# Optimization experiments

Hardware: AMD Instinct MI355X
Metric: run time of the kernel (lower is better)

## Reference

```python
import jax, jax.numpy as jnp
import numpy as np

B, L, D, K = 64, 1024, 128, 256
SQRT_2D = float(np.sqrt(2 * D))


def _biamlp(x1, x2, Wi, bi, Wq, bq):
    # proj to 2*D, norm-weighted fusion, avg-pool(2)*2 (== pairwise sum), L2-normalize over dim 1
    f1 = x1 @ Wi + bi          # [B, L, 2D]
    f2 = x2 @ Wq + bq          # [B, L, 2D]
    n1 = jnp.linalg.norm(f1)   # global L2 norm (scalar), as torch.norm(., p=2)
    n2 = jnp.linalg.norm(f2)
    e = (n1 / (n1 + n2)) * f1 + (n2 / (n1 + n2)) * f2
    b, l, c = e.shape
    z = e.reshape(b, l, c // 2, 2).mean(-1) * 2.0   # AvgPool1d(2,2) * 2 -> [B, L, D]
    denom = jnp.maximum(jnp.linalg.norm(z, axis=1, keepdims=True), 1e-12)  # F.normalize dim=1
    return z / denom


def _branch(feats, G_src, W_aff, W_c, W_lin, W_h):
    # feats: [B, L, D]; G_src: [B, L, 2D] (tensor fed to the affine projection)
    # a_j = affine(G_src^T): [B, 2D, L] @ [L, L]
    a_j = jnp.einsum('blc,lm->bcm', G_src, W_aff)            # [B, 2D, L]
    att = jnp.einsum('bld,bcl->bdc', feats, a_j) / SQRT_2D    # [B, D, 2D]
    C = jnp.tanh(att)
    H = jax.nn.relu(C @ W_c + jnp.einsum('bld,lk->bdk', feats, W_lin))  # [B, D, K]
    out = jnp.swapaxes(H @ W_h, 1, 2) + feats                 # [B, L, D]
    return out


def setup_inputs() -> dict:
    key = jax.random.key(0)
    ks = jax.random.split(key, 22)
    s = 0.02
    inp = {
        'f1_norm': jax.random.normal(ks[0], (B, L, D), jnp.float32),
        'f2_norm': jax.random.normal(ks[1], (B, L, D), jnp.float32),
        'f3_norm': jax.random.normal(ks[2], (B, L, D), jnp.float32),
        # BiAMLP params (feat_size = 128)
        'Wi': jax.random.normal(ks[3], (D, 2 * D), jnp.float32) * s,
        'bi': jax.random.normal(ks[4], (2 * D,), jnp.float32) * s,
        'Wq': jax.random.normal(ks[5], (D, 2 * D), jnp.float32) * s,
        'bq': jax.random.normal(ks[6], (2 * D,), jnp.float32) * s,
        # affine_{a,v,l}: Linear(l, l, bias=False), stored [in, out]
        'Wa_aff': jax.random.normal(ks[7], (L, L), jnp.float32) * s,
        'Wv_aff': jax.random.normal(ks[8], (L, L), jnp.float32) * s,
        'Wl_aff': jax.random.normal(ks[9], (L, L), jnp.float32) * s,
        # W_{a,v,t}: Linear(l, k)
        'W_a': jax.random.normal(ks[10], (L, K), jnp.float32) * s,
        'W_v': jax.random.normal(ks[11], (L, K), jnp.float32) * s,
        'W_t': jax.random.normal(ks[12], (L, K), jnp.float32) * s,
        # W_c{a,v,t}: Linear(2d, k)
        'W_ca': jax.random.normal(ks[13], (2 * D, K), jnp.float32) * s,
        'W_cv': jax.random.normal(ks[14], (2 * D, K), jnp.float32) * s,
        'W_ct': jax.random.normal(ks[15], (2 * D, K), jnp.float32) * s,
        # W_h{a,v,t}: Linear(k, l)
        'W_ha': jax.random.normal(ks[16], (K, L), jnp.float32) * s,
        'W_hv': jax.random.normal(ks[17], (K, L), jnp.float32) * s,
        'W_ht': jax.random.normal(ks[18], (K, L), jnp.float32) * s,
    }
    return inp


def reference(f1_norm, f2_norm, f3_norm, Wi, bi, Wq, bq, Wa_aff, Wv_aff, Wl_aff,
              W_a, W_v, W_t, W_ca, W_cv, W_ct, W_ha, W_hv, W_ht):
    txt, aud, vis = f1_norm, f2_norm, f3_norm
    # G2 = mode(txt, vis) and G3 = mode(aud, vis) are computed but unused in the
    # original (dead code); only G = G1 affects the output.
    G = _biamlp(txt, aud, Wi, bi, Wq, bq)        # [B, L, D]
    G_ag = jnp.concatenate([aud, G], axis=2)     # [B, L, 2D]
    G_lg = jnp.concatenate([txt, G], axis=2)     # [B, L, 2D]
    # NOTE: original bug preserved -- the visual branch projects G_ag (not G_vg).
    aud_out = _branch(aud, G_ag, Wa_aff, W_ca, W_a, W_ha)
    vis_out = _branch(vis, G_ag, Wv_aff, W_cv, W_v, W_hv)
    txt_out = _branch(txt, G_lg, Wl_aff, W_ct, W_t, W_ht)
    return (txt_out, aud_out, vis_out)
```

## Files before the change

### kernel.cpp

```cpp
#include <hip/hip_runtime.h>
#include <math.h>

typedef __attribute__((ext_vector_type(8))) short bf16x8;
typedef __attribute__((ext_vector_type(4))) float f32x4;

static constexpr int B_ = 64, L_ = 1024, D_ = 128, K_ = 256;
static constexpr long BLD_ = (long)B_ * L_ * D_;
static constexpr long LD_  = (long)L_ * D_;

__device__ __forceinline__ unsigned short f2b(float f) {
    unsigned int u = __builtin_bit_cast(unsigned int, f);
    u = (u + 0x7fffu + ((u >> 16) & 1u)) >> 16;
    return (unsigned short)u;
}
__device__ __forceinline__ float b2f(unsigned short h) {
    unsigned int u = ((unsigned int)h) << 16;
    return __builtin_bit_cast(float, u);
}

__device__ __forceinline__ void gl16(const unsigned short* g, unsigned short* s) {
    __builtin_amdgcn_global_load_lds(
        (const __attribute__((address_space(1))) unsigned int*)g,
        (__attribute__((address_space(3))) unsigned int*)s, 16, 0, 0);
}

struct TrEnt { const float* src; unsigned short* dst; int R, C, tr, start; };
struct TrTab { TrEnt e[17]; };

__global__ __launch_bounds__(256)
void trk(TrTab tab)
{
    __shared__ unsigned short T[64][72];
    int bid = blockIdx.x;
    int ei = 0;
    #pragma unroll
    for (int i = 1; i < 17; ++i) if (bid >= tab.e[i].start) ei = i;
    TrEnt e = tab.e[ei];
    int tile = bid - e.start;
    int ntR = e.R >> 6, ntC = e.C >> 6;
    int nt = ntR * ntC;
    int bb = tile / nt, tt = tile - bb * nt;
    int ri = tt % ntR, ci = tt / ntR;
    const float* src = e.src + (long)bb * e.R * e.C + (long)(ri * 64) * e.C + ci * 64;
    int t = threadIdx.x;
    if (!e.tr) {
        unsigned short* dstd = e.dst + (long)bb * e.R * e.C + (long)(ri * 64) * e.C + ci * 64;
        int r = t >> 2, cq = t & 3;
        const float* s = src + (long)r * e.C + cq * 16;
        unsigned short tmp[16];
        #pragma unroll
        for (int f = 0; f < 4; ++f) {
            float4 v = *(const float4*)(s + f * 4);
            tmp[f*4+0]=f2b(v.x); tmp[f*4+1]=f2b(v.y); tmp[f*4+2]=f2b(v.z); tmp[f*4+3]=f2b(v.w);
        }
        unsigned short* dp = dstd + (long)r * e.C + cq * 16;
        *(uint4*)&dp[0] = *(uint4*)&tmp[0];
        *(uint4*)&dp[8] = *(uint4*)&tmp[8];
        return;
    }
    unsigned short* dst = e.dst + (long)bb * e.R * e.C + (long)(ci * 64) * e.R + ri * 64;
    {
        int r = t >> 2, cq = t & 3;
        const float* s = src + (long)r * e.C + cq * 16;
        unsigned short tmp[16];
        #pragma unroll
        for (int f = 0; f < 4; ++f) {
            float4 v = *(const float4*)(s + f * 4);
            tmp[f*4+0]=f2b(v.x); tmp[f*4+1]=f2b(v.y); tmp[f*4+2]=f2b(v.z); tmp[f*4+3]=f2b(v.w);
        }
        *(uint4*)&T[r][cq*16]   = *(uint4*)&tmp[0];
        *(uint4*)&T[r][cq*16+8] = *(uint4*)&tmp[8];
    }
    __syncthreads();
    {
        int cr = t >> 2, rq = t & 3;
        unsigned short tmp[16];
        #pragma unroll
        for (int j = 0; j < 16; ++j) tmp[j] = T[rq*16 + j][cr];
        unsigned short* dp = dst + (long)cr * e.R + rq * 16;
        *(uint4*)&dp[0] = *(uint4*)&tmp[0];
        *(uint4*)&dp[8] = *(uint4*)&tmp[8];
    }
}

struct OpDesc {
    const unsigned short* A;
    long aOff0, aOff1, aOff2, sA;
    int lda;
    const unsigned short* B0;
    long bOff0, bOff1, bOff2, sB0;
    const unsigned short* B1;
    long sB1;
    int ldb;
    void* C;
    long sC;
    int ldc;
    const float* E0; const float* E1; const float* E2;
    float* ss;
    int Kd;
};

template<int EPI, int AF32, int TM>
__device__ __forceinline__ void gbody(const OpDesc& d, int bx, int by, int zrem,
                                      unsigned short (*As)[TM][32],
                                      unsigned short (*Bs)[128][32])
{
    const int tid = threadIdx.x;
    const long m0 = (long)bx * TM;
    const int n0 = by * 128;
    const int br = zrem >> 6, bb = zrem & 63;

    long aO = (br == 0 ? d.aOff0 : br == 1 ? d.aOff1 : d.aOff2) + (long)bb * d.sA;
    const unsigned short* A_ = d.A + aO;
    const float* Af = (const float*)d.A;
    const unsigned short* Bp;
    int nB = n0;
    if (d.B1 && n0 >= 128) { Bp = d.B1 + (long)bb * d.sB1; nB = n0 - 128; }
    else { Bp = d.B0 + (br == 0 ? d.bOff0 : br == 1 ? d.bOff1 : d.bOff2) + (long)bb * d.sB0; }

    const int w = tid >> 6, l = tid & 63;
    const int wm = (TM == 128) ? (w >> 1) : 0;
    const int wn = (TM == 128) ? (w & 1) : w;
    const int NJ = (TM == 128) ? 4 : 2;
    const int WS = (TM == 128) ? 64 : 32;
    const int fr = l & 15, kg = l >> 4;

    f32x4 acc[4][4];
    #pragma unroll
    for (int i = 0; i < 4; ++i)
        #pragma unroll
        for (int j = 0; j < 4; ++j)
            acc[i][j] = (f32x4){0.f, 0.f, 0.f, 0.f};

    const int sc8 = ((l & 3) ^ ((l >> 3) & 3)) * 8;
    const int rc  = (kg ^ ((fr >> 1) & 3)) * 8;

    auto stage = [&](int buf, int k0) {
        if (AF32) {
            int row = tid >> 1, half = tid & 1;
            const float* s = Af + (long)(m0 + row) * d.lda + k0 + half * 16;
            unsigned short tmp[16];
            #pragma unroll
            for (int f = 0; f < 4; ++f) {
                float4 v = *(const float4*)(s + f * 4);
                tmp[f*4+0]=f2b(v.x); tmp[f*4+1]=f2b(v.y); tmp[f*4+2]=f2b(v.z); tmp[f*4+3]=f2b(v.w);
            }
            int sw = (row >> 1) & 3;
            *(uint4*)&As[buf][row][((2*half    ) ^ sw) * 8] = *(uint4*)&tmp[0];
            *(uint4*)&As[buf][row][((2*half + 1) ^ sw) * 8] = *(uint4*)&tmp[8];
        } else if (TM == 128) {
            const unsigned short* ga = A_ + (m0 + 32*w + (l >> 2)) * (long)d.lda + k0 + sc8;
            gl16(ga,                    &As[buf][32*w][0]);
            gl16(ga + 16*(long)d.lda,   &As[buf][32*w + 16][0]);
        } else {
            const unsigned short* ga = A_ + (m0 + 16*w + (l >> 2)) * (long)d.lda + k0 + sc8;
            gl16(ga, &As[buf][16*w][0]);
        }
        const unsigned short* gb = Bp + (long)(nB + 32*w + (l >> 2)) * d.ldb + k0 + sc8;
        gl16(gb,                  &Bs[buf][32*w][0]);
        gl16(gb + 16*(long)d.ldb, &Bs[buf][32*w + 16][0]);
    };

    auto compute = [&](int cb) {
        bf16x8 af[4], bf[4];
        #pragma unroll
        for (int i = 0; i < 4; ++i) af[i] = *(const bf16x8*)&As[cb][wm*64 + i*16 + fr][rc];
        #pragma unroll
        for (int j = 0; j < NJ; ++j) bf[j] = *(const bf16x8*)&Bs[cb][wn*WS + j*16 + fr][rc];
        #pragma unroll
        for (int i = 0; i < 4; ++i)
            #pragma unroll
            for (int j = 0; j < NJ; ++j)
                acc[i][j] = __builtin_amdgcn_mfma_f32_16x16x32_bf16(af[i], bf[j], acc[i][j], 0, 0, 0);
    };

    const int nt = d.Kd >> 5;
    stage(0, 0);
    __syncthreads();
    for (int t = 0; t < nt; ++t) {
        if (t + 1 < nt) stage((t + 1) & 1, (t + 1) << 5);
        compute(t & 1);
        __syncthreads();
    }

    if (EPI == 4) {
        unsigned short* C = (unsigned short*)d.C;
        float lss = 0.f;
        #pragma unroll
        for (int i = 0; i < 4; ++i)
            #pragma unroll
            for (int j = 0; j < 4; ++j) {
                int cg = n0 + wn*64 + j*16 + fr;
                float bias = d.E0[cg];
                #pragma unroll
                for (int r = 0; r < 4; ++r) {
                    float v = acc[i][j][r] + bias;
                    lss += v * v;
                }
            }
        #pragma unroll
        for (int o = 32; o; o >>= 1) lss += __shfl_xor(lss, o);
        __shared__ float red4[4];
        if (l == 0) red4[w] = lss;
        float* eb = (float*)As;
        #pragma unroll
        for (int cc = 0; cc < 4; ++cc) {
            __syncthreads();
            #pragma unroll
            for (int j = 0; j < 4; ++j) {
                int cg = n0 + wn*64 + j*16 + fr;
                float bias = d.E0[cg];
                #pragma unroll
                for (int r = 0; r < 4; ++r)
                    eb[(wm*16 + kg*4 + r)*128 + wn*64 + j*16 + fr] = acc[cc][j][r] + bias;
            }
            __syncthreads();
            int lr = tid >> 3, pc = tid & 7;
            long gr = m0 + (lr < 16 ? cc*16 + lr : 48 + cc*16 + lr);
            unsigned short pk[8];
            #pragma unroll
            for (int e = 0; e < 8; ++e) {
                float v0 = eb[lr*128 + pc*16 + 2*e];
                float v1 = eb[lr*128 + pc*16 + 2*e + 1];
                pk[e] = f2b(v0 + v1);
            }
            *(uint4*)&C[gr * (long)d.ldc + (n0 >> 1) + pc*8] = *(uint4*)&pk[0];
        }
        if (tid == 0)
            d.ss[bx * 2 + by] = red4[0] + red4[1] + red4[2] + red4[3];
    } else if (TM == 64) {
        float* eb = (float*)As;
        #pragma unroll
        for (int cc = 0; cc < 4; ++cc) {
            __syncthreads();
            #pragma unroll
            for (int j = 0; j < 2; ++j)
                #pragma unroll
                for (int r = 0; r < 4; ++r)
                    eb[(kg*4 + r)*128 + wn*32 + j*16 + fr] = acc[cc][j][r];
            __syncthreads();
            unsigned short* C = (unsigned short*)d.C + (long)zrem * d.sC;
            int colx = (tid & 15) * 8;
            int lr = tid >> 4;
            long gr = m0 + cc*16 + lr;
            long gi = gr * (long)d.ldc + n0 + colx;
            unsigned short ov[8];
            if (EPI == 2) *(uint4*)ov = *(const uint4*)&C[gi];
            unsigned short pk[8];
            #pragma unroll
            for (int e = 0; e < 8; ++e) {
                float v = eb[lr*128 + colx + e];
                if (EPI == 1) v = tanhf(v * 0.0625f);
                if (EPI == 2) v = fmaxf(v + b2f(ov[e]), 0.f);
                pk[e] = f2b(v);
            }
            *(uint4*)&C[gi] = *(uint4*)&pk[0];
        }
    } else {
        float* eb = (float*)As;
        #pragma unroll
        for (int cc = 0; cc < 4; ++cc) {
            __syncthreads();
            #pragma unroll
            for (int j = 0; j < 4; ++j)
                #pragma unroll
                for (int r = 0; r < 4; ++r)
                    eb[(wm*16 + kg*4 + r)*128 + wn*64 + j*16 + fr] = acc[cc][j][r];
            __syncthreads();
            if (EPI == 3) {
                long off = (br == 2) ? 0L : (long)(br + 1) * BLD_;
                float* Co = (float*)d.C + off + (long)bb * LD_;
                const float* Ep = (br == 0 ? d.E0 : br == 1 ? d.E1 : d.E2) + (long)bb * LD_;
                int colx = (tid & 31) * 4;
                #pragma unroll
                for (int p = 0; p < 4; ++p) {
                    int lr = (tid >> 5) + 8 * p;
                    long gr = m0 + (lr < 16 ? cc*16 + lr : 48 + cc*16 + lr);
                    long gi = gr * (long)d.ldc + n0 + colx;
                    float4 v = *(float4*)&eb[lr*128 + colx];
                    float4 e4 = *(const float4*)&Ep[gi];
                    v.x += e4.x; v.y += e4.y; v.z += e4.z; v.w += e4.w;
                    *(float4*)&Co[gi] = v;
                }
            } else {
                unsigned short* C = (unsigned short*)d.C + (long)zrem * d.sC;
                int colx = (tid & 15) * 8;
                #pragma unroll
                for (int p = 0; p < 2; ++p) {
                    int lr = (tid >> 4) + 16 * p;
                    long gr = m0 + (lr < 16 ? cc*16 + lr : 48 + cc*16 + lr);
                    long gi = gr * (long)d.ldc + n0 + colx;
                    unsigned short ov[8];
                    if (EPI == 2) *(uint4*)ov = *(const uint4*)&C[gi];
                    unsigned short pk[8];
                    #pragma unroll
                    for (int e = 0; e < 8; ++e) {
                        float v = eb[lr*128 + colx + e];
                        if (EPI == 1) v = tanhf(v * 0.0625f);
                        if (EPI == 2) v = fmaxf(v + b2f(ov[e]), 0.f);
                        pk[e] = f2b(v);
                    }
                    *(uint4*)&C[gi] = *(uint4*)&pk[0];
                }
            }
        }
    }
}

template<int EPI0, int EPI1, int AF32, int SWZ, int TM>
__global__ __launch_bounds__(256)
void mg(OpDesc d0, OpDesc d1, int zsplit)
{
    __shared__ __align__(16) unsigned short As[2][TM][32];
    __shared__ __align__(16) unsigned short Bs[2][128][32];
    int bx, by, bz;
    if (SWZ) {
        int nwg = gridDim.x * gridDim.y * gridDim.z;
        int c = blockIdx.x + gridDim.x * (blockIdx.y + gridDim.y * blockIdx.z);
        int lid = (c & 7) * (nwg >> 3) + (c >> 3);
        bx = lid % gridDim.x; lid /= gridDim.x;
        by = lid % gridDim.y; bz = lid / gridDim.y;
    } else {
        bx = blockIdx.x; by = blockIdx.y; bz = blockIdx.z;
    }
    if (bz < zsplit) gbody<EPI0, AF32, TM>(d0, bx, by, bz, As, Bs);
    else             gbody<EPI1, AF32, TM>(d1, bx, by, bz - zsplit, As, Bs);
}

__global__ __launch_bounds__(256)
void k2z(unsigned short* __restrict__ q1, const unsigned short* __restrict__ q2,
         const float* __restrict__ partial, float* __restrict__ colssP)
{
    int t = threadIdx.x;
    float a = partial[t] + partial[t + 256] + partial[t + 512] + partial[t + 768];
    float bsum = partial[1024 + t] + partial[1280 + t] + partial[1536 + t] + partial[1792 + t];
    #pragma unroll
    for (int o = 32; o; o >>= 1) { a += __shfl_xor(a, o); bsum += __shfl_xor(bsum, o); }
    __shared__ float ra[4], rb[4];
    int wv = t >> 6;
    if ((t & 63) == 0) { ra[wv] = a; rb[wv] = bsum; }
    __syncthreads();
    float n1 = sqrtf(ra[0] + ra[1] + ra[2] + ra[3]);
    float n2 = sqrtf(rb[0] + rb[1] + rb[2] + rb[3]);
    float al = n1 / (n1 + n2), be = n2 / (n1 + n2);

    int b = blockIdx.x, lc = blockIdx.y;
    int d = t & 127, ls = t >> 7;
    long base = ((long)b * L_ + (long)lc * 64) * D_;
    float acc = 0.f;
    for (int ll = ls; ll < 64; ll += 2) {
        long idx = base + (long)ll * D_ + d;
        float zv = al * b2f(q1[idx]) + be * b2f(q2[idx]);
        q1[idx] = f2b(zv);
        acc += zv * zv;
    }
    __shared__ float red[256];
    red[t] = acc;
    __syncthreads();
    if (t < 128)
        colssP[((long)b * 16 + lc) * 128 + d] = red[t] + red[t + 128];
}

__global__ __launch_bounds__(256)
void k3nT(const unsigned short* __restrict__ z, const float* __restrict__ colssP,
          unsigned short* __restrict__ GT)
{
    __shared__ unsigned short T[128][136];
    int b = blockIdx.x, lt = blockIdx.y;
    int t = threadIdx.x;
    {
        int r = t >> 1, half = t & 1;
        const unsigned short* src = z + ((long)b * L_ + lt * 128 + r) * D_ + half * 64;
        #pragma unroll
        for (int q = 0; q < 8; ++q)
            *(uint4*)&T[r][half*64 + q*8] = *(const uint4*)(src + q*8);
    }
    __syncthreads();
    {
        int d = t >> 1, lh = t & 1;
        float s = 0.f;
        #pragma unroll
        for (int lc = 0; lc < 16; ++lc)
            s += colssP[((long)b * 16 + lc) * 128 + d];
        float inv = 1.f / fmaxf(sqrtf(s), 1e-12f);
        unsigned short tmp[64];
        #pragma unroll
        for (int j = 0; j < 64; ++j) tmp[j] = f2b(b2f(T[lh*64 + j][d]) * inv);
        unsigned short* dp = GT + ((long)b * D_ + d) * L_ + lt * 128 + lh * 64;
        #pragma unroll
        for (int q = 0; q < 8; ++q) *(uint4*)&dp[q*8] = *(uint4*)&tmp[q*8];
    }
}

extern "C" void kernel_launch(void* const* d_in, const int* in_sizes, int n_in,
                              void* d_out, int out_size, void* d_ws, size_t ws_size,
                              hipStream_t stream)
{
    const float* txt = (const float*)d_in[0];
    const float* aud = (const float*)d_in[1];
    const float* vis = (const float*)d_in[2];
    const float* Wi  = (const float*)d_in[3];
    const float* bi  = (const float*)d_in[4];
    const float* Wq  = (const float*)d_in[5];
    const float* bq  = (const float*)d_in[6];
    const float* Waff[3] = { (const float*)d_in[7], (const float*)d_in[8], (const float*)d_in[9] };
    const float* Wlin[3] = { (const float*)d_in[10], (const float*)d_in[11], (const float*)d_in[12] };
    const float* Wc[3]   = { (const float*)d_in[13], (const float*)d_in[14], (const float*)d_in[15] };
    const float* Wh[3]   = { (const float*)d_in[16], (const float*)d_in[17], (const float*)d_in[18] };

    unsigned short* w16 = (unsigned short*)d_ws;
    unsigned short* featT = w16;
    unsigned short* q1b   = featT + 3 * BLD_;
    unsigned short* q2b   = q1b + BLD_;
    unsigned short* WAb   = q2b + BLD_;
    unsigned short* WLTb  = WAb + 3145728;
    unsigned short* WCTb  = WLTb + 786432;
    unsigned short* WHTb  = WCTb + 196608;
    unsigned short* WiTb  = WHTb + 786432;
    unsigned short* WqTb  = WiTb + 32768;
    float* partial = (float*)(WqTb + 32768);
    float* colssP  = partial + 2048;
    unsigned short* Cm3 = q1b;
    unsigned short* Hb3 = q1b + 6291456;
    unsigned short* S2all = (unsigned short*)d_out;
    unsigned short* GT    = S2all + 3 * BLD_;

    TrTab tab;
    auto setE = [&](int i, const float* s, unsigned short* dst, int R, int C, int tr, int start) {
        tab.e[i].src = s; tab.e[i].dst = dst; tab.e[i].R = R; tab.e[i].C = C;
        tab.e[i].tr = tr; tab.e[i].start = start;
    };
    int st = 0;
    setE(0, aud, featT + 0,        1024, 128, 1, st); st += 2048;
    setE(1, vis, featT + BLD_,     1024, 128, 1, st); st += 2048;
    setE(2, txt, featT + 2 * BLD_, 1024, 128, 1, st); st += 2048;
    setE(3, Wi, WiTb, 128, 256, 1, st); st += 8;
    setE(4, Wq, WqTb, 128, 256, 1, st); st += 8;
    for (int i = 0; i < 3; ++i) { setE(5 + i, Wlin[i], WLTb + (long)i * 262144, 1024, 256, 1, st); st += 64; }
    for (int i = 0; i < 3; ++i) { setE(8 + i, Wc[i],   WCTb + (long)i * 65536,  256, 256, 1, st); st += 16; }
    for (int i = 0; i < 3; ++i) { setE(11 + i, Wh[i],  WHTb + (long)i * 262144, 256, 1024, 1, st); st += 64; }
    for (int i = 0; i < 3; ++i) { setE(14 + i, Waff[i], WAb + (long)i * 1048576, 1024, 1024, 0, st); st += 256; }
    trk<<<st, 256, 0, stream>>>(tab);

    OpDesc dTxt = {}, dAud = {};
    dTxt.A = (const unsigned short*)txt; dTxt.lda = 128;
    dTxt.B0 = WiTb; dTxt.ldb = 128;
    dTxt.C = q1b; dTxt.ldc = 128;
    dTxt.E0 = bi; dTxt.ss = partial; dTxt.Kd = 128;
    dAud = dTxt;
    dAud.A = (const unsigned short*)aud; dAud.B0 = WqTb; dAud.C = q2b;
    dAud.E0 = bq; dAud.ss = partial + 1024;
    mg<4, 4, 1, 0, 128><<<dim3(512, 2, 2), 256, 0, stream>>>(dTxt, dAud, 1);

    k2z<<<dim3(64, 16), 256, 0, stream>>>(q1b, q2b, partial, colssP);
    k3nT<<<dim3(64, 8), 256, 0, stream>>>(q1b, colssP, GT);

    OpDesc dS2 = {};
    dS2.A = featT; dS2.aOff0 = 0; dS2.aOff1 = BLD_; dS2.aOff2 = 2 * BLD_;
    dS2.sA = LD_; dS2.lda = 1024;
    dS2.B0 = WAb; dS2.bOff0 = 0; dS2.bOff1 = 1048576; dS2.bOff2 = 2097152;
    dS2.sB0 = 0; dS2.ldb = 1024;
    dS2.C = S2all; dS2.sC = LD_; dS2.ldc = 1024; dS2.Kd = 1024;
    mg<0, 0, 0, 1, 128><<<dim3(1, 8, 192), 256, 0, stream>>>(dS2, dS2, 192);

    OpDesc dAtt = {};
    dAtt.A = S2all; dAtt.aOff0 = 0; dAtt.aOff1 = 64 * LD_; dAtt.aOff2 = 128 * LD_;
    dAtt.sA = LD_; dAtt.lda = 1024;
    dAtt.B0 = featT; dAtt.bOff0 = 0; dAtt.bOff1 = 0; dAtt.bOff2 = 2 * BLD_;
    dAtt.sB0 = LD_;
    dAtt.B1 = GT; dAtt.sB1 = LD_; dAtt.ldb = 1024;
    dAtt.C = Cm3; dAtt.sC = 32768; dAtt.ldc = 256; dAtt.Kd = 1024;
    OpDesc dU = {};
    dU.A = featT; dU.aOff0 = 0; dU.aOff1 = BLD_; dU.aOff2 = 2 * BLD_;
    dU.sA = LD_; dU.lda = 1024;
    dU.B0 = WLTb; dU.bOff0 = 0; dU.bOff1 = 262144; dU.bOff2 = 524288;
    dU.sB0 = 0; dU.ldb = 1024;
    dU.C = Hb3; dU.sC = 32768; dU.ldc = 256; dU.Kd = 1024;
    mg<1, 0, 0, 1, 64><<<dim3(2, 2, 384), 256, 0, stream>>>(dAtt, dU, 192);

    OpDesc dT = {};
    dT.A = Cm3; dT.aOff0 = 0; dT.aOff1 = 2097152; dT.aOff2 = 4194304;
    dT.sA = 32768; dT.lda = 256;
    dT.B0 = WCTb; dT.bOff0 = 0; dT.bOff1 = 65536; dT.bOff2 = 131072;
    dT.sB0 = 0; dT.ldb = 256;
    dT.C = Hb3; dT.sC = 32768; dT.ldc = 256; dT.Kd = 256;
    mg<2, 2, 0, 1, 64><<<dim3(2, 2, 192), 256, 0, stream>>>(dT, dT, 192);

    OpDesc dOut = {};
    dOut.A = WHTb; dOut.aOff0 = 0; dOut.aOff1 = 262144; dOut.aOff2 = 524288;
    dOut.sA = 0; dOut.lda = 256;
    dOut.B0 = Hb3; dOut.bOff0 = 0; dOut.bOff1 = 2097152; dOut.bOff2 = 4194304;
    dOut.sB0 = 32768; dOut.ldb = 256;
    dOut.C = d_out; dOut.ldc = 128;
    dOut.E0 = aud; dOut.E1 = vis; dOut.E2 = txt; dOut.Kd = 256;
    mg<3, 3, 0, 1, 128><<<dim3(8, 1, 192), 256, 0, stream>>>(dOut, dOut, 192);
}
```

Before: 296.7 us.

## Triple-buffer LDS staging with vmcnt waits in bf16 GEMM main loop

For the bf16-input GEMM path, the double-buffered loop with a full __syncthreads per K-step becomes a three-stage LDS ring. Two tiles are prefetched ahead, and explicit s_waitcnt vmcnt plus a bare s_barrier wait only for the current tile's async global_load_lds. The aim is to hide more global-load latency and avoid draining all outstanding loads each iteration. In exchange it uses 50% more shared memory, which may reduce occupancy, and it relies on hand-counted vmcnt values per tile size.

```diff
diff --git a/kernel.cpp b/kernel.cpp
--- a/kernel.cpp
+++ b/kernel.cpp
@@ -100,7 +100,7 @@
     int Kd;
 };
 
-template<int EPI, int AF32, int TM>
+template<int EPI, int AF32, int TM, int NBUF>
 __device__ __forceinline__ void gbody(const OpDesc& d, int bx, int by, int zrem,
                                       unsigned short (*As)[TM][32],
                                       unsigned short (*Bs)[128][32])
@@ -175,11 +175,34 @@
     };
 
     const int nt = d.Kd >> 5;
-    stage(0, 0);
-    __syncthreads();
-    for (int t = 0; t < nt; ++t) {
-        if (t + 1 < nt) stage((t + 1) & 1, (t + 1) << 5);
-        compute(t & 1);
+    if (AF32) {
+        stage(0, 0);
+        __syncthreads();
+        for (int t = 0; t < nt; ++t) {
+            if (t + 1 < nt) stage((t + 1) & 1, (t + 1) << 5);
+            compute(t & 1);
+            __syncthreads();
+        }
+    } else {
+        stage(0, 0);
+        stage(1, 32);
+        int cb = 0, sb = 2;
+        for (int t = 0; t < nt; ++t) {
+            if (t + 1 < nt) {
+                if (TM == 128) asm volatile("s_waitcnt vmcnt(4)" ::: "memory");
+                else           asm volatile("s_waitcnt vmcnt(3)" ::: "memory");
+            } else {
+                asm volatile("s_waitcnt vmcnt(0)" ::: "memory");
+            }
+            __builtin_amdgcn_s_barrier();
+            __builtin_amdgcn_sched_barrier(0);
+            if (t + 2 < nt) {
+                stage(sb, (t + 2) << 5);
+                sb = (sb == 2) ? 0 : sb + 1;
+            }
+            compute(cb);
+            cb = (cb == 2) ? 0 : cb + 1;
+        }
         __syncthreads();
     }
 
@@ -311,8 +334,9 @@
 __global__ __launch_bounds__(256)
 void mg(OpDesc d0, OpDesc d1, int zsplit)
 {
-    __shared__ __align__(16) unsigned short As[2][TM][32];
-    __shared__ __align__(16) unsigned short Bs[2][128][32];
+    constexpr int NBUF = AF32 ? 2 : 3;
+    __shared__ __align__(16) unsigned short As[NBUF][TM][32];
+    __shared__ __align__(16) unsigned short Bs[NBUF][128][32];
     int bx, by, bz;
     if (SWZ) {
         int nwg = gridDim.x * gridDim.y * gridDim.z;
@@ -323,8 +347,8 @@
     } else {
         bx = blockIdx.x; by = blockIdx.y; bz = blockIdx.z;
     }
-    if (bz < zsplit) gbody<EPI0, AF32, TM>(d0, bx, by, bz, As, Bs);
-    else             gbody<EPI1, AF32, TM>(d1, bx, by, bz - zsplit, As, Bs);
+    if (bz < zsplit) gbody<EPI0, AF32, TM, NBUF>(d0, bx, by, bz, As, Bs);
+    else             gbody<EPI1, AF32, TM, NBUF>(d1, bx, by, bz - zsplit, As, Bs);
 }
 
 __global__ __launch_bounds__(256)
```

Result: no change. 296.1 us (-0.2%).
